# Performance work log

Measured on AMD Instinct MI355X. Metric: run time of the kernel, lower is better.

The kernel has to match this reference:

```python
import jax, jax.numpy as jnp
import numpy as np

D_MODEL = 1024
HEADS = 16
D_HEAD = D_MODEL // HEADS


def setup_inputs() -> dict:
    key = jax.random.key(0)
    ks = jax.random.split(key, 7)
    s = 1.0 / np.sqrt(D_MODEL)
    x = jax.random.normal(ks[0], (4, 2048, D_MODEL), dtype=jnp.float32)
    Wq = jax.random.uniform(ks[1], (D_MODEL, D_MODEL), jnp.float32, -s, s)
    bq = jax.random.uniform(ks[2], (D_MODEL,), jnp.float32, -s, s)
    Wk = jax.random.uniform(ks[3], (D_MODEL, D_MODEL), jnp.float32, -s, s)
    bk = jax.random.uniform(ks[4], (D_MODEL,), jnp.float32, -s, s)
    Wv = jax.random.uniform(ks[5], (D_MODEL, D_MODEL), jnp.float32, -s, s)
    bv = jax.random.uniform(ks[6], (D_MODEL,), jnp.float32, -s, s)
    return {"x": x, "Wq": Wq, "bq": bq, "Wk": Wk, "bk": bk, "Wv": Wv, "bv": bv}


def reference(x, Wq, bq, Wk, bk, Wv, bv):
    B, S, D = x.shape
    # QKV projections, split heads: [B, H, S, Dh]
    def split(t):
        return t.reshape(B, S, HEADS, D_HEAD).transpose(0, 2, 1, 3)
    q = split(x @ Wq + bq)
    k = split(x @ Wk + bk)
    v = split(x @ Wv + bv)
    scores = jnp.einsum('bhqd,bhkd->bhqk', q, k) / np.sqrt(D_HEAD).astype(jnp.float32)
    attn = jax.nn.softmax(scores, axis=-1)
    out = jnp.einsum('bhqk,bhkd->bhqd', attn, v)
    return out.transpose(0, 2, 1, 3).reshape(B, S, D)
```

## Files before the change

### kernel.cpp

```cpp
#include <hip/hip_runtime.h>

typedef _Float16 f16;
typedef __attribute__((ext_vector_type(2))) _Float16 f16x2;
typedef __attribute__((ext_vector_type(2))) __fp16   hf16x2;
typedef __attribute__((ext_vector_type(4))) _Float16 f16x4;
typedef __attribute__((ext_vector_type(8))) _Float16 f16x8;
typedef __attribute__((ext_vector_type(4))) float    f32x4;

#define D_MODEL 1024
#define HEADS   16
#define DH      64
#define SEQ     2048
#define BATCH   4
#define SSCALE  0.1803368801111204f

__device__ __forceinline__ void gload_lds16(const void* g, void* lds) {
  __builtin_amdgcn_global_load_lds(
      (const __attribute__((address_space(1))) unsigned int*)g,
      (__attribute__((address_space(3))) unsigned int*)lds, 16, 0, 0);
}

__global__ __launch_bounds__(256) void prep_kernel(const float* __restrict__ x,
                                                   const float* __restrict__ Wq,
                                                   const float* __restrict__ Wk,
                                                   const float* __restrict__ Wv,
                                                   f16* __restrict__ xb,
                                                   f16* __restrict__ wt) {
  if (blockIdx.x < 8192) {
    int i = blockIdx.x * 256 + threadIdx.x;
    float4 v = ((const float4*)x)[i];
    f16x4 h;
    h[0] = (f16)v.x; h[1] = (f16)v.y; h[2] = (f16)v.z; h[3] = (f16)v.w;
    ((f16x4*)xb)[i] = h;
    return;
  }
  int bid = blockIdx.x - 8192;
  int z = bid >> 8, rem = bid & 255;
  const float* W = z == 0 ? Wq : (z == 1 ? Wk : Wv);
  f16* out = wt + (size_t)z * D_MODEL * D_MODEL;
  __shared__ float tile[64][65];
  int n0 = (rem & 15) * 64, k0 = (rem >> 4) * 64;
  int tx = threadIdx.x & 63, ty = threadIdx.x >> 6;
#pragma unroll
  for (int r = 0; r < 16; ++r)
    tile[ty * 16 + r][tx] = W[(size_t)(k0 + ty * 16 + r) * D_MODEL + n0 + tx];
  __syncthreads();
#pragma unroll
  for (int r = 0; r < 16; ++r)
    out[(size_t)(n0 + ty * 16 + r) * D_MODEL + k0 + tx] = (f16)tile[tx][ty * 16 + r];
}

__global__ __launch_bounds__(256, 3) void qkv_gemm_kernel(
    const f16* __restrict__ xb, const f16* __restrict__ wt_all,
    const float* __restrict__ bq, const float* __restrict__ bk, const float* __restrict__ bv,
    f16* __restrict__ qout, f16* __restrict__ kout, f16* __restrict__ vtout) {
  const int z = blockIdx.z;
  const f16* wt = wt_all + (size_t)z * D_MODEL * D_MODEL;
  const float* bias = z == 0 ? bq : (z == 1 ? bk : bv);
  const int n0 = blockIdx.x * 128, m0 = blockIdx.y * 128;

  __shared__ f16 As[2][128 * 32];
  __shared__ f16 Bs[2][128 * 32];

  const int tid = threadIdx.x;
  const int lane = tid & 63, w = tid >> 6;
  const int quad = lane >> 4, l15 = lane & 15;
  const int wm = w & 1, wn = w >> 1;

  const int pce = (quad ^ ((l15 >> 1) & 3)) * 8;
  const int aoff = wm * 2048 + l15 * 32 + pce;
  const int boff = wn * 2048 + l15 * 32 + pce;

  int srow[2], scl[2];
#pragma unroll
  for (int c = 0; c < 2; ++c) {
    int slot = (w * 2 + c) * 64 + lane;
    srow[c] = slot >> 2;
    scl[c] = (slot & 3) ^ ((srow[c] >> 1) & 3);
  }

  f32x4 acc[4][4];
#pragma unroll
  for (int i = 0; i < 4; ++i)
#pragma unroll
    for (int j = 0; j < 4; ++j) acc[i][j] = (f32x4){0.f, 0.f, 0.f, 0.f};

#pragma unroll
  for (int c = 0; c < 2; ++c) {
    gload_lds16(xb + (size_t)(m0 + srow[c]) * D_MODEL + scl[c] * 8, &As[0][(w * 2 + c) * 512]);
    gload_lds16(wt + (size_t)(n0 + srow[c]) * D_MODEL + scl[c] * 8, &Bs[0][(w * 2 + c) * 512]);
  }

  for (int k0 = 0; k0 < D_MODEL; k0 += 32) {
    const int buf = (k0 >> 5) & 1;
    const int kn = (k0 + 32) & (D_MODEL - 1);
    __syncthreads();
#pragma unroll
    for (int c = 0; c < 2; ++c) {
      gload_lds16(xb + (size_t)(m0 + srow[c]) * D_MODEL + kn + scl[c] * 8, &As[buf ^ 1][(w * 2 + c) * 512]);
      gload_lds16(wt + (size_t)(n0 + srow[c]) * D_MODEL + kn + scl[c] * 8, &Bs[buf ^ 1][(w * 2 + c) * 512]);
    }
    f16x8 a[4], b[4];
#pragma unroll
    for (int mt = 0; mt < 4; ++mt) a[mt] = *(const f16x8*)(&As[buf][aoff + mt * 512]);
#pragma unroll
    for (int nt = 0; nt < 4; ++nt) b[nt] = *(const f16x8*)(&Bs[buf][boff + nt * 512]);
#pragma unroll
    for (int mt = 0; mt < 4; ++mt)
#pragma unroll
      for (int nt = 0; nt < 4; ++nt)
        acc[mt][nt] = __builtin_amdgcn_mfma_f32_16x16x32_f16(a[mt], b[nt], acc[mt][nt], 0, 0, 0);
  }

  const float sc = (z == 0) ? SSCALE : 1.0f;
  float bcol[4];
#pragma unroll
  for (int nt = 0; nt < 4; ++nt) bcol[nt] = bias[n0 + wn * 64 + nt * 16 + l15];

  if (z < 2) {
    f16* out = (z == 0) ? qout : kout;
#pragma unroll
    for (int mt = 0; mt < 4; ++mt) {
      int mbase = m0 + wm * 64 + mt * 16 + quad * 4;
#pragma unroll
      for (int nt = 0; nt < 4; ++nt) {
        int n = n0 + wn * 64 + nt * 16 + l15;
        int h = n >> 6, dh = n & 63;
#pragma unroll
        for (int r = 0; r < 4; ++r) {
          int m = mbase + r;
          int b = m >> 11, s = m & 2047;
          out[((size_t)(b * HEADS + h) * SEQ + s) * DH + dh] = (f16)((acc[mt][nt][r] + bcol[nt]) * sc);
        }
      }
    }
  } else {
#pragma unroll
    for (int mt = 0; mt < 4; ++mt) {
      int mbase = m0 + wm * 64 + mt * 16 + quad * 4;
      int b = mbase >> 11, s = mbase & 2047;
#pragma unroll
      for (int nt = 0; nt < 4; ++nt) {
        int n = n0 + wn * 64 + nt * 16 + l15;
        int h = n >> 6, dh = n & 63;
        f16x4 v;
#pragma unroll
        for (int r = 0; r < 4; ++r) v[r] = (f16)(acc[mt][nt][r] + bcol[nt]);
        *(f16x4*)(vtout + ((size_t)(b * HEADS + h) * DH + dh) * SEQ + s) = v;
      }
    }
  }
}

__global__ __launch_bounds__(256, 4) void attn_kernel(
    const f16* __restrict__ q, const f16* __restrict__ k, const f16* __restrict__ vt,
    float* __restrict__ out) {
  const int bh = blockIdx.x;
  const int s0 = blockIdx.y * 128;
  const int b = bh >> 4, h = bh & 15;
  const int tid = threadIdx.x, lane = tid & 63, w = tid >> 6;
  const int quad = lane >> 4, l15 = lane & 15;
  const int qh = quad >> 1, q1 = quad & 1;

  __shared__ f16 Ks[2][64 * 64];
  __shared__ f16 Vs[2][64 * 64];

  const f16* qbase = q + ((size_t)bh * SEQ + s0 + w * 32) * DH;
  const f16* kbase = k + (size_t)bh * SEQ * DH;
  const f16* vbase = vt + (size_t)bh * DH * SEQ;

  f16x8 qf[2][2];
#pragma unroll
  for (int qt = 0; qt < 2; ++qt)
#pragma unroll
    for (int ks = 0; ks < 2; ++ks)
      qf[qt][ks] = *(const f16x8*)(qbase + (qt * 16 + l15) * DH + ks * 32 + quad * 8);

  int koff[2];
  koff[0] = l15 * 64 + ((quad ^ (l15 & 7)) * 8);
  koff[1] = l15 * 64 + (((4 + quad) ^ (l15 & 7)) * 8);
  int voff[4];
#pragma unroll
  for (int ks = 0; ks < 4; ++ks)
    voff[ks] = l15 * 64 + (((ks * 2 + qh) ^ (l15 & 7)) * 8) + q1 * 4;

  int srow[2], scl[2];
#pragma unroll
  for (int c = 0; c < 2; ++c) {
    int slot = (w * 2 + c) * 64 + lane;
    srow[c] = slot >> 3;
    scl[c] = (slot & 7) ^ (srow[c] & 7);
  }

  float lsum[2] = {0.f, 0.f};
  f32x4 o[4][2];
#pragma unroll
  for (int i = 0; i < 4; ++i)
#pragma unroll
    for (int j = 0; j < 2; ++j) o[i][j] = (f32x4){0.f, 0.f, 0.f, 0.f};

#pragma unroll
  for (int c = 0; c < 2; ++c) {
    gload_lds16(kbase + (size_t)srow[c] * DH + scl[c] * 8, &Ks[0][(w * 2 + c) * 512]);
    gload_lds16(vbase + (size_t)srow[c] * SEQ + scl[c] * 8, &Vs[0][(w * 2 + c) * 512]);
  }

  for (int kt = 0; kt < SEQ / 64; ++kt) {
    const int buf = kt & 1;
    const int ktn = (kt + 1) & (SEQ / 64 - 1);
    __syncthreads();
#pragma unroll
    for (int c = 0; c < 2; ++c) {
      gload_lds16(kbase + (size_t)(ktn * 64 + srow[c]) * DH + scl[c] * 8, &Ks[buf ^ 1][(w * 2 + c) * 512]);
      gload_lds16(vbase + (size_t)srow[c] * SEQ + ktn * 64 + scl[c] * 8, &Vs[buf ^ 1][(w * 2 + c) * 512]);
    }

    f32x4 st[4][2];
#pragma unroll
    for (int mt = 0; mt < 4; ++mt)
#pragma unroll
      for (int qt = 0; qt < 2; ++qt) st[mt][qt] = (f32x4){0.f, 0.f, 0.f, 0.f};
#pragma unroll
    for (int mt = 0; mt < 4; ++mt)
#pragma unroll
      for (int ks = 0; ks < 2; ++ks) {
        f16x8 af = *(const f16x8*)(&Ks[buf][koff[ks] + mt * 1024]);
#pragma unroll
        for (int qt = 0; qt < 2; ++qt)
          st[mt][qt] = __builtin_amdgcn_mfma_f32_16x16x32_f16(af, qf[qt][ks], st[mt][qt], 0, 0, 0);
      }

#pragma unroll
    for (int ks = 0; ks < 4; ++ks) {
      f16x4 pb[2];
#pragma unroll
      for (int qt = 0; qt < 2; ++qt) {
        float e0 = __builtin_amdgcn_exp2f(st[ks][qt][0]);
        float e1 = __builtin_amdgcn_exp2f(st[ks][qt][1]);
        float e2 = __builtin_amdgcn_exp2f(st[ks][qt][2]);
        float e3 = __builtin_amdgcn_exp2f(st[ks][qt][3]);
        lsum[qt] += (e0 + e1) + (e2 + e3);
        f16x2 p01 = __builtin_bit_cast(f16x2, __builtin_amdgcn_cvt_pkrtz(e0, e1));
        f16x2 p23 = __builtin_bit_cast(f16x2, __builtin_amdgcn_cvt_pkrtz(e2, e3));
        pb[qt] = __builtin_shufflevector(p01, p23, 0, 1, 2, 3);
      }
#pragma unroll
      for (int mt = 0; mt < 4; ++mt) {
        f16x4 va = *(const f16x4*)(&Vs[buf][voff[ks] + mt * 1024]);
#pragma unroll
        for (int qt = 0; qt < 2; ++qt)
          o[mt][qt] = __builtin_amdgcn_mfma_f32_16x16x16f16(va, pb[qt], o[mt][qt], 0, 0, 0);
      }
    }
  }

#pragma unroll
  for (int qt = 0; qt < 2; ++qt) {
    float l = lsum[qt];
    l += __shfl_xor(l, 16, 64);
    l += __shfl_xor(l, 32, 64);
    float inv = 1.f / l;
    int sq = s0 + w * 32 + qt * 16 + l15;
    float* obase = out + ((size_t)b * SEQ + sq) * D_MODEL + h * DH;
#pragma unroll
    for (int mt = 0; mt < 4; ++mt) {
      f32x4 vv;
#pragma unroll
      for (int r = 0; r < 4; ++r) vv[r] = o[mt][qt][r] * inv;
      *(f32x4*)(obase + mt * 16 + quad * 4) = vv;
    }
  }
}

extern "C" void kernel_launch(void* const* d_in, const int* in_sizes, int n_in,
                              void* d_out, int out_size, void* d_ws, size_t ws_size,
                              hipStream_t stream) {
  const float* x  = (const float*)d_in[0];
  const float* Wq = (const float*)d_in[1];
  const float* bq = (const float*)d_in[2];
  const float* Wk = (const float*)d_in[3];
  const float* bk = (const float*)d_in[4];
  const float* Wv = (const float*)d_in[5];
  const float* bv = (const float*)d_in[6];
  float* out = (float*)d_out;

  char* ws = (char*)d_ws;
  f16* xb = (f16*)ws;
  f16* wt = (f16*)(ws + (size_t)16 * 1024 * 1024);
  f16* q  = (f16*)(ws + (size_t)22 * 1024 * 1024);
  f16* kk = q + (size_t)BATCH * SEQ * D_MODEL;
  f16* vt = kk + (size_t)BATCH * SEQ * D_MODEL;

  prep_kernel<<<8192 + 768, 256, 0, stream>>>(x, Wq, Wk, Wv, xb, wt);
  qkv_gemm_kernel<<<dim3(8, 64, 3), 256, 0, stream>>>(xb, wt, bq, bk, bv, q, kk, vt);
  attn_kernel<<<dim3(64, 16), 256, 0, stream>>>(q, kk, vt, out);
}
```

Measured before the change: 265.3 us.

## Software-pipeline MFMA against LDS loads in projection and attention kernels

In the projection GEMM, fragments read from LDS are held in registers and multiplied on the next iteration, so the LDS reads of the current tile overlap the MFMAs of the previous one. In attention, the P·V product for the previous key tile is deferred one iteration so it overlaps the QK^T MFMAs and exp work of the current tile, using a triple-buffered V in LDS with a rotating index. The wrap-around prefetch on the last iteration is also removed. The cost is more registers for the carried fragments and probabilities, plus extra LDS for the third V buffer, which may lower occupancy under launch_bounds(256,4).

```diff
diff --git a/kernel.cpp b/kernel.cpp
--- a/kernel.cpp
+++ b/kernel.cpp
@@ -91,26 +91,38 @@
     gload_lds16(wt + (size_t)(n0 + srow[c]) * D_MODEL + scl[c] * 8, &Bs[0][(w * 2 + c) * 512]);
   }
 
-  for (int k0 = 0; k0 < D_MODEL; k0 += 32) {
-    const int buf = (k0 >> 5) & 1;
-    const int kn = (k0 + 32) & (D_MODEL - 1);
+  f16x8 aP[4], bP[4];
+  for (int it = 0; it < 32; ++it) {
+    const int buf = it & 1;
     __syncthreads();
-#pragma unroll
-    for (int c = 0; c < 2; ++c) {
-      gload_lds16(xb + (size_t)(m0 + srow[c]) * D_MODEL + kn + scl[c] * 8, &As[buf ^ 1][(w * 2 + c) * 512]);
-      gload_lds16(wt + (size_t)(n0 + srow[c]) * D_MODEL + kn + scl[c] * 8, &Bs[buf ^ 1][(w * 2 + c) * 512]);
-    }
-    f16x8 a[4], b[4];
-#pragma unroll
-    for (int mt = 0; mt < 4; ++mt) a[mt] = *(const f16x8*)(&As[buf][aoff + mt * 512]);
-#pragma unroll
-    for (int nt = 0; nt < 4; ++nt) b[nt] = *(const f16x8*)(&Bs[buf][boff + nt * 512]);
-#pragma unroll
-    for (int mt = 0; mt < 4; ++mt)
-#pragma unroll
-      for (int nt = 0; nt < 4; ++nt)
-        acc[mt][nt] = __builtin_amdgcn_mfma_f32_16x16x32_f16(a[mt], b[nt], acc[mt][nt], 0, 0, 0);
-  }
+    if (it < 31) {
+      const int kn = (it + 1) * 32;
+#pragma unroll
+      for (int c = 0; c < 2; ++c) {
+        gload_lds16(xb + (size_t)(m0 + srow[c]) * D_MODEL + kn + scl[c] * 8, &As[buf ^ 1][(w * 2 + c) * 512]);
+        gload_lds16(wt + (size_t)(n0 + srow[c]) * D_MODEL + kn + scl[c] * 8, &Bs[buf ^ 1][(w * 2 + c) * 512]);
+      }
+    }
+    f16x8 aC[4], bC[4];
+#pragma unroll
+    for (int mt = 0; mt < 4; ++mt) aC[mt] = *(const f16x8*)(&As[buf][aoff + mt * 512]);
+#pragma unroll
+    for (int nt = 0; nt < 4; ++nt) bC[nt] = *(const f16x8*)(&Bs[buf][boff + nt * 512]);
+    if (it) {
+#pragma unroll
+      for (int mt = 0; mt < 4; ++mt)
+#pragma unroll
+        for (int nt = 0; nt < 4; ++nt)
+          acc[mt][nt] = __builtin_amdgcn_mfma_f32_16x16x32_f16(aP[mt], bP[nt], acc[mt][nt], 0, 0, 0);
+    }
+#pragma unroll
+    for (int t = 0; t < 4; ++t) { aP[t] = aC[t]; bP[t] = bC[t]; }
+  }
+#pragma unroll
+  for (int mt = 0; mt < 4; ++mt)
+#pragma unroll
+    for (int nt = 0; nt < 4; ++nt)
+      acc[mt][nt] = __builtin_amdgcn_mfma_f32_16x16x32_f16(aP[mt], bP[nt], acc[mt][nt], 0, 0, 0);
 
   const float sc = (z == 0) ? SSCALE : 1.0f;
   float bcol[4];
@@ -163,7 +175,7 @@
   const int qh = quad >> 1, q1 = quad & 1;
 
   __shared__ f16 Ks[2][64 * 64];
-  __shared__ f16 Vs[2][64 * 64];
+  __shared__ f16 Vs[3][64 * 64];
 
   const f16* qbase = q + ((size_t)bh * SEQ + s0 + w * 32) * DH;
   const f16* kbase = k + (size_t)bh * SEQ * DH;
@@ -198,6 +210,7 @@
   for (int i = 0; i < 4; ++i)
 #pragma unroll
     for (int j = 0; j < 2; ++j) o[i][j] = (f32x4){0.f, 0.f, 0.f, 0.f};
+  const f32x4 Zero = (f32x4){0.f, 0.f, 0.f, 0.f};
 
 #pragma unroll
   for (int c = 0; c < 2; ++c) {
@@ -205,34 +218,47 @@
     gload_lds16(vbase + (size_t)srow[c] * SEQ + scl[c] * 8, &Vs[0][(w * 2 + c) * 512]);
   }
 
+  f16x4 pbP[4][2];
+  int vb = 0, vbn = 1, vbp = 2;
+
   for (int kt = 0; kt < SEQ / 64; ++kt) {
-    const int buf = kt & 1;
-    const int ktn = (kt + 1) & (SEQ / 64 - 1);
+    const int kb = kt & 1;
     __syncthreads();
-#pragma unroll
-    for (int c = 0; c < 2; ++c) {
-      gload_lds16(kbase + (size_t)(ktn * 64 + srow[c]) * DH + scl[c] * 8, &Ks[buf ^ 1][(w * 2 + c) * 512]);
-      gload_lds16(vbase + (size_t)srow[c] * SEQ + ktn * 64 + scl[c] * 8, &Vs[buf ^ 1][(w * 2 + c) * 512]);
+    if (kt < SEQ / 64 - 1) {
+      const int kn = (kt + 1) * 64;
+#pragma unroll
+      for (int c = 0; c < 2; ++c) {
+        gload_lds16(kbase + (size_t)(kn + srow[c]) * DH + scl[c] * 8, &Ks[kb ^ 1][(w * 2 + c) * 512]);
+        gload_lds16(vbase + (size_t)srow[c] * SEQ + kn + scl[c] * 8, &Vs[vbn][(w * 2 + c) * 512]);
+      }
     }
 
     f32x4 st[4][2];
 #pragma unroll
-    for (int mt = 0; mt < 4; ++mt)
-#pragma unroll
-      for (int qt = 0; qt < 2; ++qt) st[mt][qt] = (f32x4){0.f, 0.f, 0.f, 0.f};
-#pragma unroll
-    for (int mt = 0; mt < 4; ++mt)
-#pragma unroll
-      for (int ks = 0; ks < 2; ++ks) {
-        f16x8 af = *(const f16x8*)(&Ks[buf][koff[ks] + mt * 1024]);
-#pragma unroll
-        for (int qt = 0; qt < 2; ++qt)
-          st[mt][qt] = __builtin_amdgcn_mfma_f32_16x16x32_f16(af, qf[qt][ks], st[mt][qt], 0, 0, 0);
-      }
-
-#pragma unroll
-    for (int ks = 0; ks < 4; ++ks) {
-      f16x4 pb[2];
+    for (int mt = 0; mt < 4; ++mt) {
+      f16x8 af0 = *(const f16x8*)(&Ks[kb][koff[0] + mt * 1024]);
+      f16x8 af1 = *(const f16x8*)(&Ks[kb][koff[1] + mt * 1024]);
+#pragma unroll
+      for (int qt = 0; qt < 2; ++qt) {
+        st[mt][qt] = __builtin_amdgcn_mfma_f32_16x16x32_f16(af0, qf[qt][0], Zero, 0, 0, 0);
+        st[mt][qt] = __builtin_amdgcn_mfma_f32_16x16x32_f16(af1, qf[qt][1], st[mt][qt], 0, 0, 0);
+      }
+    }
+
+    if (kt) {
+#pragma unroll
+      for (int ks = 0; ks < 4; ++ks)
+#pragma unroll
+        for (int mt = 0; mt < 4; ++mt) {
+          f16x4 va = *(const f16x4*)(&Vs[vbp][voff[ks] + mt * 1024]);
+#pragma unroll
+          for (int qt = 0; qt < 2; ++qt)
+            o[mt][qt] = __builtin_amdgcn_mfma_f32_16x16x16f16(va, pbP[ks][qt], o[mt][qt], 0, 0, 0);
+        }
+    }
+
+#pragma unroll
+    for (int ks = 0; ks < 4; ++ks)
 #pragma unroll
       for (int qt = 0; qt < 2; ++qt) {
         float e0 = __builtin_amdgcn_exp2f(st[ks][qt][0]);
@@ -242,17 +268,21 @@
         lsum[qt] += (e0 + e1) + (e2 + e3);
         f16x2 p01 = __builtin_bit_cast(f16x2, __builtin_amdgcn_cvt_pkrtz(e0, e1));
         f16x2 p23 = __builtin_bit_cast(f16x2, __builtin_amdgcn_cvt_pkrtz(e2, e3));
-        pb[qt] = __builtin_shufflevector(p01, p23, 0, 1, 2, 3);
-      }
-#pragma unroll
-      for (int mt = 0; mt < 4; ++mt) {
-        f16x4 va = *(const f16x4*)(&Vs[buf][voff[ks] + mt * 1024]);
-#pragma unroll
-        for (int qt = 0; qt < 2; ++qt)
-          o[mt][qt] = __builtin_amdgcn_mfma_f32_16x16x16f16(va, pb[qt], o[mt][qt], 0, 0, 0);
-      }
-    }
-  }
+        pbP[ks][qt] = __builtin_shufflevector(p01, p23, 0, 1, 2, 3);
+      }
+
+    int t = vbp; vbp = vb; vb = vbn; vbn = t;
+  }
+
+#pragma unroll
+  for (int ks = 0; ks < 4; ++ks)
+#pragma unroll
+    for (int mt = 0; mt < 4; ++mt) {
+      f16x4 va = *(const f16x4*)(&Vs[vbp][voff[ks] + mt * 1024]);
+#pragma unroll
+      for (int qt = 0; qt < 2; ++qt)
+        o[mt][qt] = __builtin_amdgcn_mfma_f32_16x16x16f16(va, pbP[ks][qt], o[mt][qt], 0, 0, 0);
+    }
 
 #pragma unroll
   for (int qt = 0; qt < 2; ++qt) {
```

Measured after the change: 283.1 us. 1.07x slower.
